# Optimization experiments

Hardware: AMD Instinct MI355X
Metric: run time of the kernel (lower is better)

Reference implementation:

```python
import jax, jax.numpy as jnp
import numpy as np

N_DENSE = 13
N_SPARSE = 26
SPARSE_DIM = 100                       # all sparse vocab sizes equal
N_FIELD = N_DENSE + N_SPARSE           # 39
N_FEATURES = N_DENSE + N_SPARSE * SPARSE_DIM  # 2613
K = 16
BATCH = 16384


def setup_inputs() -> dict:
    key = jax.random.key(0)
    k1, k2, k3, k4, k5 = jax.random.split(key, 5)
    dense = jax.random.normal(k1, (BATCH, N_DENSE), dtype=jnp.float32)
    sparse = jax.random.randint(k2, (BATCH, N_SPARSE), 0, SPARSE_DIM).astype(jnp.float32)
    x = jnp.concatenate([dense, sparse], axis=1)  # [B, 39]
    # nn.Linear(n_features, 1) params
    lim = 1.0 / np.sqrt(N_FEATURES)
    w_weight = jax.random.uniform(k3, (1, N_FEATURES), jnp.float32, -lim, lim)
    w_bias = jax.random.uniform(k4, (1,), jnp.float32, -lim, lim)
    # v initialized to zeros in the module; use small randn so grads are nontrivial
    v = jax.random.normal(k5, (N_FEATURES, N_FIELD, K), dtype=jnp.float32) * 0.01
    return {"x": x, "w_weight": w_weight, "w_bias": w_bias, "v": v}


def _build_inputs(x):
    dense_x = x[:, :N_DENSE]                             # [B, 13]
    sparse_x = x[:, N_DENSE:].astype(jnp.int32)          # [B, 26]
    oh = jax.nn.one_hot(sparse_x, SPARSE_DIM, dtype=jnp.float32)  # [B, 26, 100]
    return jnp.concatenate([dense_x, oh.reshape(x.shape[0], -1)], axis=1)  # [B, 2613]


def reference(x, w_weight, w_bias, v):
    inputs = _build_inputs(x)                            # [B, n_features]
    linear_part = inputs @ w_weight.T + w_bias           # [B, 1]
    field_f = jnp.einsum('bn,nfk->bfk', inputs, v)       # [B, n_field, k]
    # sum_{i<j} <f_i, f_j> = 0.5 * ((sum_f)^2 - sum_f f^2), summed over k
    s = jnp.sum(field_f, axis=1)                         # [B, k]
    sq = jnp.sum(field_f * field_f, axis=1)              # [B, k]
    cross_part = 0.5 * jnp.sum(s * s - sq, axis=1, keepdims=True)  # [B, 1]
    return jax.nn.sigmoid(linear_part + cross_part)
```

## Files before the change

### kernel.cpp

```cpp
#include <hip/hip_runtime.h>
#include <hip/hip_fp16.h>
#include <math.h>

#define N_DENSE 13
#define N_SPARSE 26
#define SPARSE_DIM 100
#define N_FIELD 39
#define KDIM 16
#define N_FEATURES 2613
#define ROW_F 624
#define ROW_DW 320
#define ROW_U2 160
#define THREADS 256
#define ROWS_PER_BLOCK 4

#define CVT_TOTAL (N_FEATURES * ROW_U2)
__global__ __launch_bounds__(256) void cvt_pad_f16v(
    const float* __restrict__ v, uint2* __restrict__ o)
{
    int stride = gridDim.x * blockDim.x;
    for (int i = blockIdx.x * blockDim.x + threadIdx.x; i < CVT_TOTAL; i += stride) {
        int n = i / ROW_U2;
        int r = i - n * ROW_U2;
        uint2 w2 = make_uint2(0u, 0u);
        int e = 4 * r;
        if (e < ROW_F) {
            float4 f = *reinterpret_cast<const float4*>(v + (size_t)n * ROW_F + e);
            __half2 h0 = __floats2half2_rn(f.x, f.y);
            __half2 h1 = __floats2half2_rn(f.z, f.w);
            w2.x = *reinterpret_cast<unsigned int*>(&h0);
            w2.y = *reinterpret_cast<unsigned int*>(&h1);
        }
        o[(size_t)n * ROW_U2 + r] = w2;
    }
}

__global__ __launch_bounds__(THREADS, 7) void ffm_f16u(
    const float* __restrict__ x,
    const float* __restrict__ w,
    const float* __restrict__ bias,
    const __half2* __restrict__ vb,
    float* __restrict__ out,
    int B)
{
    __shared__ __half2 ldsDense[N_DENSE * ROW_DW];
    {
        const uint4* src = reinterpret_cast<const uint4*>(vb);
        uint4* dst = reinterpret_cast<uint4*>(ldsDense);
        for (int i = threadIdx.x; i < N_DENSE * ROW_DW / 4; i += THREADS)
            dst[i] = src[i];
    }
    __syncthreads();

    const int l = threadIdx.x & 63;
    const int wv = __builtin_amdgcn_readfirstlane((int)(threadIdx.x >> 6));
    const int row = blockIdx.x * ROWS_PER_BLOCK + wv;
    if (row >= B) return;

    const float* xr = x + (size_t)row * N_FIELD;

    __half2 acc[5];
#pragma unroll
    for (int m = 0; m < 5; ++m) acc[m] = __floats2half2_rn(0.f, 0.f);

    float lin = bias[0];

#pragma unroll
    for (int j = 0; j < N_DENSE; ++j) {
        float xv = xr[j];
        lin = fmaf(xv, w[j], lin);
        __half2 xh = __float2half2_rn(xv);
#pragma unroll
        for (int m = 0; m < 5; ++m)
            acc[m] = __hfma2(xh, ldsDense[j * ROW_DW + 64 * m + l], acc[m]);
    }

#pragma unroll
    for (int s = 0; s < 24; s += 4) {
        int i0 = N_DENSE + (s    ) * SPARSE_DIM + (int)xr[N_DENSE + s    ];
        int i1 = N_DENSE + (s + 1) * SPARSE_DIM + (int)xr[N_DENSE + s + 1];
        int i2 = N_DENSE + (s + 2) * SPARSE_DIM + (int)xr[N_DENSE + s + 2];
        int i3 = N_DENSE + (s + 3) * SPARSE_DIM + (int)xr[N_DENSE + s + 3];
        const __half2* b0 = vb + (size_t)i0 * ROW_DW + l;
        const __half2* b1 = vb + (size_t)i1 * ROW_DW + l;
        const __half2* b2 = vb + (size_t)i2 * ROW_DW + l;
        const __half2* b3 = vb + (size_t)i3 * ROW_DW + l;
        __half2 t00 = b0[0], t01 = b0[64], t02 = b0[128], t03 = b0[192], t04 = b0[256];
        __half2 t10 = b1[0], t11 = b1[64], t12 = b1[128], t13 = b1[192], t14 = b1[256];
        __half2 t20 = b2[0], t21 = b2[64], t22 = b2[128], t23 = b2[192], t24 = b2[256];
        __half2 t30 = b3[0], t31 = b3[64], t32 = b3[128], t33 = b3[192], t34 = b3[256];
        lin += w[i0] + w[i1] + w[i2] + w[i3];
        acc[0] = __hadd2(acc[0], t00); acc[1] = __hadd2(acc[1], t01);
        acc[2] = __hadd2(acc[2], t02); acc[3] = __hadd2(acc[3], t03);
        acc[4] = __hadd2(acc[4], t04);
        acc[0] = __hadd2(acc[0], t10); acc[1] = __hadd2(acc[1], t11);
        acc[2] = __hadd2(acc[2], t12); acc[3] = __hadd2(acc[3], t13);
        acc[4] = __hadd2(acc[4], t14);
        acc[0] = __hadd2(acc[0], t20); acc[1] = __hadd2(acc[1], t21);
        acc[2] = __hadd2(acc[2], t22); acc[3] = __hadd2(acc[3], t23);
        acc[4] = __hadd2(acc[4], t24);
        acc[0] = __hadd2(acc[0], t30); acc[1] = __hadd2(acc[1], t31);
        acc[2] = __hadd2(acc[2], t32); acc[3] = __hadd2(acc[3], t33);
        acc[4] = __hadd2(acc[4], t34);
    }
    {
        int i0 = N_DENSE + 24 * SPARSE_DIM + (int)xr[N_DENSE + 24];
        int i1 = N_DENSE + 25 * SPARSE_DIM + (int)xr[N_DENSE + 25];
        const __half2* b0 = vb + (size_t)i0 * ROW_DW + l;
        const __half2* b1 = vb + (size_t)i1 * ROW_DW + l;
        __half2 t00 = b0[0], t01 = b0[64], t02 = b0[128], t03 = b0[192], t04 = b0[256];
        __half2 t10 = b1[0], t11 = b1[64], t12 = b1[128], t13 = b1[192], t14 = b1[256];
        lin += w[i0] + w[i1];
        acc[0] = __hadd2(acc[0], t00); acc[1] = __hadd2(acc[1], t01);
        acc[2] = __hadd2(acc[2], t02); acc[3] = __hadd2(acc[3], t03);
        acc[4] = __hadd2(acc[4], t04);
        acc[0] = __hadd2(acc[0], t10); acc[1] = __hadd2(acc[1], t11);
        acc[2] = __hadd2(acc[2], t12); acc[3] = __hadd2(acc[3], t13);
        acc[4] = __hadd2(acc[4], t14);
    }

    float sx = 0.f, sy = 0.f, qx = 0.f, qy = 0.f;
#pragma unroll
    for (int m = 0; m < 5; ++m) {
        float ax = __low2float(acc[m]);
        float ay = __high2float(acc[m]);
        sx += ax; sy += ay;
        qx = fmaf(ax, ax, qx);
        qy = fmaf(ay, ay, qy);
    }
#pragma unroll
    for (int mask = 8; mask <= 32; mask <<= 1) {
        sx += __shfl_xor(sx, mask);
        sy += __shfl_xor(sy, mask);
        qx += __shfl_xor(qx, mask);
        qy += __shfl_xor(qy, mask);
    }
    float c = (sx * sx - qx) + (sy * sy - qy);
    c += __shfl_xor(c, 1);
    c += __shfl_xor(c, 2);
    c += __shfl_xor(c, 4);

    float logit = lin + 0.5f * c;
    if (l == 0) out[row] = 1.f / (1.f + expf(-logit));
}

#define ROW_Q (ROW_F / 4)
__global__ __launch_bounds__(256) void ffm_fp32(
    const float* __restrict__ x, const float* __restrict__ w,
    const float* __restrict__ bias, const float* __restrict__ v,
    float* __restrict__ out, int B)
{
    __shared__ float ldsDense[N_DENSE * ROW_F];
    const float4* v4 = reinterpret_cast<const float4*>(v);
    float4* lds4 = reinterpret_cast<float4*>(ldsDense);
    for (int i = threadIdx.x; i < N_DENSE * ROW_Q; i += 256) lds4[i] = v4[i];
    __syncthreads();

    const int g = threadIdx.x >> 4, l = threadIdx.x & 15;
    const int row = blockIdx.x * 16 + g;
    if (row >= B) return;
    const float* xr = x + row * (N_DENSE + N_SPARSE);

    float4 acc[10];
#pragma unroll
    for (int i = 0; i < 10; ++i) acc[i] = make_float4(0.f, 0.f, 0.f, 0.f);
#pragma unroll
    for (int j = 0; j < N_DENSE; ++j) {
        float xv = xr[j];
        const float4* b = lds4 + j * ROW_Q;
#pragma unroll
        for (int i = 0; i < 10; ++i)
            if (i < 9 || l < 12) {
                float4 tt = b[l + 16 * i];
                acc[i].x += xv * tt.x; acc[i].y += xv * tt.y;
                acc[i].z += xv * tt.z; acc[i].w += xv * tt.w;
            }
    }
    int nidx[N_SPARSE];
#pragma unroll
    for (int s = 0; s < N_SPARSE; ++s)
        nidx[s] = N_DENSE + s * SPARSE_DIM + (int)xr[N_DENSE + s];
    for (int s = 0; s < N_SPARSE; ++s) {
        const float4* b = v4 + (size_t)nidx[s] * ROW_Q;
#pragma unroll
        for (int i = 0; i < 10; ++i)
            if (i < 9 || l < 12) {
                float4 tt = b[l + 16 * i];
                acc[i].x += tt.x; acc[i].y += tt.y; acc[i].z += tt.z; acc[i].w += tt.w;
            }
    }
    float4 s4 = make_float4(0,0,0,0), q4 = make_float4(0,0,0,0);
#pragma unroll
    for (int i = 0; i < 10; ++i) {
        s4.x += acc[i].x; s4.y += acc[i].y; s4.z += acc[i].z; s4.w += acc[i].w;
        q4.x += acc[i].x*acc[i].x; q4.y += acc[i].y*acc[i].y;
        q4.z += acc[i].z*acc[i].z; q4.w += acc[i].w*acc[i].w;
    }
#pragma unroll
    for (int m = 4; m <= 8; m <<= 1) {
        s4.x += __shfl_xor(s4.x,m); s4.y += __shfl_xor(s4.y,m);
        s4.z += __shfl_xor(s4.z,m); s4.w += __shfl_xor(s4.w,m);
        q4.x += __shfl_xor(q4.x,m); q4.y += __shfl_xor(q4.y,m);
        q4.z += __shfl_xor(q4.z,m); q4.w += __shfl_xor(q4.w,m);
    }
    float c = (s4.x*s4.x - q4.x) + (s4.y*s4.y - q4.y) +
              (s4.z*s4.z - q4.z) + (s4.w*s4.w - q4.w);
    c += __shfl_xor(c,1); c += __shfl_xor(c,2);
    float lin = bias[0];
#pragma unroll
    for (int j = 0; j < N_DENSE; ++j) lin += xr[j]*w[j];
#pragma unroll
    for (int s = 0; s < N_SPARSE; ++s) lin += w[nidx[s]];
    float logit = lin + 0.5f*c;
    if (l == 0) out[row] = 1.f/(1.f+expf(-logit));
}

extern "C" void kernel_launch(void* const* d_in, const int* in_sizes, int n_in,
                              void* d_out, int out_size, void* d_ws, size_t ws_size,
                              hipStream_t stream) {
    const float* x    = (const float*)d_in[0];
    const float* w    = (const float*)d_in[1];
    const float* bias = (const float*)d_in[2];
    const float* v    = (const float*)d_in[3];
    float* out = (float*)d_out;

    int B = in_sizes[0] / (N_DENSE + N_SPARSE);
    size_t need = (size_t)N_FEATURES * ROW_DW * sizeof(__half2);

    if (ws_size >= need) {
        int cvt_grid = (CVT_TOTAL + 255) / 256;
        cvt_pad_f16v<<<cvt_grid, 256, 0, stream>>>(v, (uint2*)d_ws);
        int grid = (B + ROWS_PER_BLOCK - 1) / ROWS_PER_BLOCK;
        ffm_f16u<<<grid, THREADS, 0, stream>>>(
            x, w, bias, (const __half2*)d_ws, out, B);
    } else {
        int grid = (B + 15) / 16;
        ffm_fp32<<<grid, 256, 0, stream>>>(x, w, bias, v, out, B);
    }
}
```

Measured before the change: 36.44 us.

## Precompute sparse byte offsets and linear term in prep kernel alongside table conversion

The conversion kernel is extended with extra blocks that, per row, compute the linear term and the byte offsets of the 26 sparse embedding rows into workspace. The main kernel then reads precomputed offsets and the linear value instead of converting floats to indices and gathering w itself. This is meant to shorten the main kernel's critical path and hide the index and linear work inside the already required prep launch. It adds workspace traffic, writing and rereading about 1.7 MB of indices plus the linear values.

```diff
diff --git a/kernel.cpp b/kernel.cpp
--- a/kernel.cpp
+++ b/kernel.cpp
@@ -11,34 +11,57 @@
 #define ROW_F 624
 #define ROW_DW 320
 #define ROW_U2 160
+#define ROW_BYTES 1280
 #define THREADS 256
 #define ROWS_PER_BLOCK 4
 
 #define CVT_TOTAL (N_FEATURES * ROW_U2)
-__global__ __launch_bounds__(256) void cvt_pad_f16v(
-    const float* __restrict__ v, uint2* __restrict__ o)
+#define CVT_BLOCKS ((CVT_TOTAL + 255) / 256)
+__global__ __launch_bounds__(256) void prep_k(
+    const float* __restrict__ v, const float* __restrict__ x,
+    const float* __restrict__ w, const float* __restrict__ bias,
+    uint2* __restrict__ table, unsigned int* __restrict__ idxb,
+    float* __restrict__ linb, int B)
 {
-    int stride = gridDim.x * blockDim.x;
-    for (int i = blockIdx.x * blockDim.x + threadIdx.x; i < CVT_TOTAL; i += stride) {
-        int n = i / ROW_U2;
-        int r = i - n * ROW_U2;
-        uint2 w2 = make_uint2(0u, 0u);
-        int e = 4 * r;
-        if (e < ROW_F) {
-            float4 f = *reinterpret_cast<const float4*>(v + (size_t)n * ROW_F + e);
-            __half2 h0 = __floats2half2_rn(f.x, f.y);
-            __half2 h1 = __floats2half2_rn(f.z, f.w);
-            w2.x = *reinterpret_cast<unsigned int*>(&h0);
-            w2.y = *reinterpret_cast<unsigned int*>(&h1);
+    int bid = blockIdx.x;
+    if (bid < CVT_BLOCKS) {
+        int i = bid * 256 + threadIdx.x;
+        if (i < CVT_TOTAL) {
+            int n = i / ROW_U2;
+            int r = i - n * ROW_U2;
+            uint2 w2 = make_uint2(0u, 0u);
+            int e = 4 * r;
+            if (e < ROW_F) {
+                float4 f = *reinterpret_cast<const float4*>(v + (size_t)n * ROW_F + e);
+                __half2 h0 = __floats2half2_rn(f.x, f.y);
+                __half2 h1 = __floats2half2_rn(f.z, f.w);
+                w2.x = *reinterpret_cast<unsigned int*>(&h0);
+                w2.y = *reinterpret_cast<unsigned int*>(&h1);
+            }
+            table[(size_t)n * ROW_U2 + r] = w2;
         }
-        o[(size_t)n * ROW_U2 + r] = w2;
-    }
-}
-
-__global__ __launch_bounds__(THREADS, 7) void ffm_f16u(
+    } else {
+        int row = (bid - CVT_BLOCKS) * 256 + threadIdx.x;
+        if (row < B) {
+            const float* xr = x + (size_t)row * N_FIELD;
+            float lin = bias[0];
+#pragma unroll
+            for (int j = 0; j < N_DENSE; ++j) lin = fmaf(xr[j], w[j], lin);
+#pragma unroll
+            for (int s = 0; s < N_SPARSE; ++s) {
+                int idx = N_DENSE + s * SPARSE_DIM + (int)xr[N_DENSE + s];
+                lin += w[idx];
+                idxb[(size_t)row * N_SPARSE + s] = (unsigned int)(idx * ROW_BYTES);
+            }
+            linb[row] = lin;
+        }
+    }
+}
+
+__global__ __launch_bounds__(THREADS, 7) void ffm_v13(
     const float* __restrict__ x,
-    const float* __restrict__ w,
-    const float* __restrict__ bias,
+    const unsigned int* __restrict__ idxb,
+    const float* __restrict__ linb,
     const __half2* __restrict__ vb,
     float* __restrict__ out,
     int B)
@@ -57,19 +80,18 @@
     const int row = blockIdx.x * ROWS_PER_BLOCK + wv;
     if (row >= B) return;
 
+    const unsigned int* idxr = idxb + (size_t)row * N_SPARSE;
+    const float lin = linb[row];
+    const char* vbp = reinterpret_cast<const char*>(vb);
+
+    __half2 acc[5];
+#pragma unroll
+    for (int m = 0; m < 5; ++m) acc[m] = __floats2half2_rn(0.f, 0.f);
+
     const float* xr = x + (size_t)row * N_FIELD;
-
-    __half2 acc[5];
-#pragma unroll
-    for (int m = 0; m < 5; ++m) acc[m] = __floats2half2_rn(0.f, 0.f);
-
-    float lin = bias[0];
-
 #pragma unroll
     for (int j = 0; j < N_DENSE; ++j) {
-        float xv = xr[j];
-        lin = fmaf(xv, w[j], lin);
-        __half2 xh = __float2half2_rn(xv);
+        __half2 xh = __float2half2_rn(xr[j]);
 #pragma unroll
         for (int m = 0; m < 5; ++m)
             acc[m] = __hfma2(xh, ldsDense[j * ROW_DW + 64 * m + l], acc[m]);
@@ -77,19 +99,14 @@
 
 #pragma unroll
     for (int s = 0; s < 24; s += 4) {
-        int i0 = N_DENSE + (s    ) * SPARSE_DIM + (int)xr[N_DENSE + s    ];
-        int i1 = N_DENSE + (s + 1) * SPARSE_DIM + (int)xr[N_DENSE + s + 1];
-        int i2 = N_DENSE + (s + 2) * SPARSE_DIM + (int)xr[N_DENSE + s + 2];
-        int i3 = N_DENSE + (s + 3) * SPARSE_DIM + (int)xr[N_DENSE + s + 3];
-        const __half2* b0 = vb + (size_t)i0 * ROW_DW + l;
-        const __half2* b1 = vb + (size_t)i1 * ROW_DW + l;
-        const __half2* b2 = vb + (size_t)i2 * ROW_DW + l;
-        const __half2* b3 = vb + (size_t)i3 * ROW_DW + l;
+        const __half2* b0 = reinterpret_cast<const __half2*>(vbp + idxr[s    ]) + l;
+        const __half2* b1 = reinterpret_cast<const __half2*>(vbp + idxr[s + 1]) + l;
+        const __half2* b2 = reinterpret_cast<const __half2*>(vbp + idxr[s + 2]) + l;
+        const __half2* b3 = reinterpret_cast<const __half2*>(vbp + idxr[s + 3]) + l;
         __half2 t00 = b0[0], t01 = b0[64], t02 = b0[128], t03 = b0[192], t04 = b0[256];
         __half2 t10 = b1[0], t11 = b1[64], t12 = b1[128], t13 = b1[192], t14 = b1[256];
         __half2 t20 = b2[0], t21 = b2[64], t22 = b2[128], t23 = b2[192], t24 = b2[256];
         __half2 t30 = b3[0], t31 = b3[64], t32 = b3[128], t33 = b3[192], t34 = b3[256];
-        lin += w[i0] + w[i1] + w[i2] + w[i3];
         acc[0] = __hadd2(acc[0], t00); acc[1] = __hadd2(acc[1], t01);
         acc[2] = __hadd2(acc[2], t02); acc[3] = __hadd2(acc[3], t03);
         acc[4] = __hadd2(acc[4], t04);
@@ -104,13 +121,10 @@
         acc[4] = __hadd2(acc[4], t34);
     }
     {
-        int i0 = N_DENSE + 24 * SPARSE_DIM + (int)xr[N_DENSE + 24];
-        int i1 = N_DENSE + 25 * SPARSE_DIM + (int)xr[N_DENSE + 25];
-        const __half2* b0 = vb + (size_t)i0 * ROW_DW + l;
-        const __half2* b1 = vb + (size_t)i1 * ROW_DW + l;
+        const __half2* b0 = reinterpret_cast<const __half2*>(vbp + idxr[24]) + l;
+        const __half2* b1 = reinterpret_cast<const __half2*>(vbp + idxr[25]) + l;
         __half2 t00 = b0[0], t01 = b0[64], t02 = b0[128], t03 = b0[192], t04 = b0[256];
         __half2 t10 = b1[0], t11 = b1[64], t12 = b1[128], t13 = b1[192], t14 = b1[256];
-        lin += w[i0] + w[i1];
         acc[0] = __hadd2(acc[0], t00); acc[1] = __hadd2(acc[1], t01);
         acc[2] = __hadd2(acc[2], t02); acc[3] = __hadd2(acc[3], t03);
         acc[4] = __hadd2(acc[4], t04);
@@ -225,14 +239,23 @@
     float* out = (float*)d_out;
 
     int B = in_sizes[0] / (N_DENSE + N_SPARSE);
-    size_t need = (size_t)N_FEATURES * ROW_DW * sizeof(__half2);
+    size_t tbl_bytes = (size_t)N_FEATURES * ROW_DW * sizeof(__half2);
+    size_t idx_bytes = (size_t)B * N_SPARSE * sizeof(unsigned int);
+    size_t lin_bytes = (size_t)B * sizeof(float);
+    size_t need = tbl_bytes + idx_bytes + lin_bytes;
 
     if (ws_size >= need) {
-        int cvt_grid = (CVT_TOTAL + 255) / 256;
-        cvt_pad_f16v<<<cvt_grid, 256, 0, stream>>>(v, (uint2*)d_ws);
+        char* wsb = (char*)d_ws;
+        uint2* table        = (uint2*)wsb;
+        unsigned int* idxb  = (unsigned int*)(wsb + tbl_bytes);
+        float* linb         = (float*)(wsb + tbl_bytes + idx_bytes);
+
+        int prep_grid = CVT_BLOCKS + (B + 255) / 256;
+        prep_k<<<prep_grid, 256, 0, stream>>>(v, x, w, bias, table, idxb, linb, B);
+
         int grid = (B + ROWS_PER_BLOCK - 1) / ROWS_PER_BLOCK;
-        ffm_f16u<<<grid, THREADS, 0, stream>>>(
-            x, w, bias, (const __half2*)d_ws, out, B);
+        ffm_v13<<<grid, THREADS, 0, stream>>>(
+            x, idxb, linb, (const __half2*)table, out, B);
     } else {
         int grid = (B + 15) / 16;
         ffm_fp32<<<grid, 256, 0, stream>>>(x, w, bias, v, out, B);
```

Result: slower. 38.57 us (+5.8%).
